# Optimization experiments

Measured on AMD Instinct MI355X. Metric: run time of the kernel, lower is better.

Reference implementation:

```python
import jax, jax.numpy as jnp
import numpy as np

INPUT_DIM = 512
EMBED_DIM = 64
B, S = 4, 4096


def setup_inputs() -> dict:
    key = jax.random.key(0)
    ks = jax.random.split(key, 9)
    scale = 1.0 / np.sqrt(INPUT_DIM)
    return {
        "q": jax.random.normal(ks[0], (B, S, INPUT_DIM), dtype=jnp.float32),
        "k": jax.random.normal(ks[1], (B, S, INPUT_DIM), dtype=jnp.float32),
        "v": jax.random.normal(ks[2], (B, S, INPUT_DIM), dtype=jnp.float32),
        "Wq": jax.random.uniform(ks[3], (INPUT_DIM, EMBED_DIM), jnp.float32, -scale, scale),
        "bq": jax.random.uniform(ks[4], (EMBED_DIM,), jnp.float32, -scale, scale),
        "Wk": jax.random.uniform(ks[5], (INPUT_DIM, EMBED_DIM), jnp.float32, -scale, scale),
        "bk": jax.random.uniform(ks[6], (EMBED_DIM,), jnp.float32, -scale, scale),
        "Wv": jax.random.uniform(ks[7], (INPUT_DIM, EMBED_DIM), jnp.float32, -scale, scale),
        "bv": jax.random.uniform(ks[8], (EMBED_DIM,), jnp.float32, -scale, scale),
    }


def reference(q, k, v, Wq, bq, Wk, bk, Wv, bv):
    # Linear projections (torch Linear: x @ W^T + b; here W stored as [in, out])
    Q = q @ Wq + bq  # [B, S, E]
    K = k @ Wk + bk  # [B, S, E]
    V = v @ Wv + bv  # [B, S, E]
    d_k = K.shape[-1]
    scores = jnp.einsum("bqe,bke->bqk", Q, K) / jnp.sqrt(jnp.float32(d_k))  # [B, S, S]
    attn = jax.nn.softmax(scores, axis=-1)
    return jnp.einsum("bqk,bke->bqe", attn, V)  # [B, S, E]
```

## Files before the change

### kernel.cpp

```cpp
#include <hip/hip_runtime.h>
#include <math.h>

#define S_ 4096
#define C_SCALE 0.18033688011112042f
#define KSPLIT 8

typedef __attribute__((ext_vector_type(4))) float  floatx4;
typedef __attribute__((ext_vector_type(4))) short  short4_t;
typedef __attribute__((ext_vector_type(8))) short  short8_t;
typedef __attribute__((ext_vector_type(4))) unsigned int uintx4;

__device__ __forceinline__ short f2bf(float f) {
  unsigned u = __builtin_bit_cast(unsigned, f);
  u += 0x7FFFu + ((u >> 16) & 1u);
  return (short)(u >> 16);
}
__device__ __forceinline__ unsigned pack2(float lo, float hi) {
  unsigned a = __builtin_bit_cast(unsigned, lo) + 0x8000u;
  unsigned b = __builtin_bit_cast(unsigned, hi) + 0x8000u;
  return __builtin_amdgcn_perm(b, a, 0x07060302u);
}
__device__ __forceinline__ unsigned packt(float lo, float hi) {
  return __builtin_amdgcn_perm(__builtin_bit_cast(unsigned, hi),
                               __builtin_bit_cast(unsigned, lo), 0x07060302u);
}
__device__ __forceinline__ float bf2f(short s) {
  return __builtin_bit_cast(float, (unsigned)((unsigned short)s) << 16);
}

__global__ __launch_bounds__(256) void prep_w(const float* __restrict__ Wq,
                                              const float* __restrict__ Wk,
                                              const float* __restrict__ Wv,
                                              short* __restrict__ Wt) {
  __shared__ float T[64 * 65];
  int m = blockIdx.x >> 3, kt = blockIdx.x & 7, tid = threadIdx.x;
  const float* W = (m == 0) ? Wq : (m == 1) ? Wk : Wv;
  float sc = (m == 0) ? C_SCALE : 1.0f;
#pragma unroll
  for (int i = 0; i < 16; i++) {
    int e = i * 256 + tid;
    int k = e >> 6, n = e & 63;
    T[k * 65 + n] = W[(kt * 64 + k) * 64 + n];
  }
  __syncthreads();
#pragma unroll
  for (int i = 0; i < 16; i++) {
    int e = i * 256 + tid;
    int n = e >> 6, k = e & 63;
    Wt[m * 32768 + n * 512 + kt * 64 + k] = f2bf(T[k * 65 + n] * sc);
  }
}

__global__ __launch_bounds__(256, 3) void proj_kernel(
    const float* __restrict__ qin, const float* __restrict__ kin,
    const float* __restrict__ vin, const float* __restrict__ bq,
    const float* __restrict__ bk, const float* __restrict__ bv,
    const short* __restrict__ Wt, short* __restrict__ Qp,
    short* __restrict__ Kp, short* __restrict__ Vt) {
  __shared__ short A_lds[2][64 * 64];

  int tid = threadIdx.x;
  int m = blockIdx.x >> 8;
  int r0 = (blockIdx.x & 255) * 64;
  int wid = tid >> 6, lane = tid & 63, l15 = lane & 15, quad = lane >> 4;

  const float* in = (m == 0) ? qin : (m == 1) ? kin : vin;
  const short* Wm = Wt + m * 32768;

  short8_t wf[8][2];
#pragma unroll
  for (int kc = 0; kc < 8; kc++)
#pragma unroll
    for (int eh = 0; eh < 2; eh++)
      wf[kc][eh] = *(const short8_t*)(Wm + (wid * 16 + l15) * 512 + kc * 64 +
                                      eh * 32 + quad * 8);

  int sr = tid >> 3, sc = tid & 7;
  int sphys = (sc ^ (sr & 7)) * 8;

  floatx4 ar[4];
  auto loadA = [&](int kc) {
    const float* p = in + (size_t)(r0 + sr) * 512 + kc * 64 + sc * 8;
    ar[0] = *(const floatx4*)p;
    ar[1] = *(const floatx4*)(p + 4);
    const float* p2 = p + 32 * 512;
    ar[2] = *(const floatx4*)p2;
    ar[3] = *(const floatx4*)(p2 + 4);
  };

  floatx4 acc[4];
#pragma unroll
  for (int rt = 0; rt < 4; rt++) acc[rt] = (floatx4){0.f, 0.f, 0.f, 0.f};

  loadA(0);
#pragma unroll
  for (int kc = 0; kc < 8; kc++) {
    uintx4 w0 = {pack2(ar[0][0], ar[0][1]), pack2(ar[0][2], ar[0][3]),
                 pack2(ar[1][0], ar[1][1]), pack2(ar[1][2], ar[1][3])};
    uintx4 w1 = {pack2(ar[2][0], ar[2][1]), pack2(ar[2][2], ar[2][3]),
                 pack2(ar[3][0], ar[3][1]), pack2(ar[3][2], ar[3][3])};
    short* Ab = &A_lds[kc & 1][0];
    *(short8_t*)(Ab + sr * 64 + sphys) = __builtin_bit_cast(short8_t, w0);
    *(short8_t*)(Ab + (sr + 32) * 64 + sphys) = __builtin_bit_cast(short8_t, w1);
    __syncthreads();
    if (kc < 7) loadA(kc + 1);
    int akey = l15 & 7;
#pragma unroll
    for (int rt = 0; rt < 4; rt++) {
      int arow = rt * 16 + l15;
#pragma unroll
      for (int eh = 0; eh < 2; eh++) {
        short8_t af = *(const short8_t*)(Ab + arow * 64 + ((eh * 4 + quad) ^ akey) * 8);
        acc[rt] = __builtin_amdgcn_mfma_f32_16x16x32_bf16(af, wf[kc][eh], acc[rt], 0, 0, 0);
      }
    }
  }

  const float* bias = (m == 0) ? bq : (m == 1) ? bk : bv;
  float bsc = (m == 0) ? C_SCALE : 1.0f;
  float bv_ = bias[wid * 16 + l15] * bsc;
  if (m < 2) {
    short* out = (m == 0) ? Qp : Kp;
#pragma unroll
    for (int rt = 0; rt < 4; rt++)
#pragma unroll
      for (int r = 0; r < 4; r++)
        out[(size_t)(r0 + rt * 16 + quad * 4 + r) * 64 + wid * 16 + l15] =
            f2bf(acc[rt][r] + bv_);
  } else {
    int bb = r0 >> 12;
    int s0 = (r0 & 4095);
#pragma unroll
    for (int rt = 0; rt < 4; rt++) {
      short4_t pk = {f2bf(acc[rt][0] + bv_), f2bf(acc[rt][1] + bv_),
                     f2bf(acc[rt][2] + bv_), f2bf(acc[rt][3] + bv_)};
      *(short4_t*)(Vt + (size_t)bb * 262144 + (wid * 16 + l15) * 4096 + s0 +
                   rt * 16 + quad * 4) = pk;
    }
  }
}

__global__ __launch_bounds__(256, 2) void attn_kernel(
    const short* __restrict__ Qp, const short* __restrict__ Kp,
    const short* __restrict__ Vt, short* __restrict__ Po,
    float* __restrict__ Lp) {
  __shared__ short K_lds[2][64 * 64];
  __shared__ short V_lds[2][64 * 64];

  int tid = threadIdx.x;
  int ks = blockIdx.x >> 6, b = (blockIdx.x >> 4) & 3, qt = blockIdx.x & 15;
  int wid = tid >> 6, lane = tid & 63, l15 = lane & 15, quad = lane >> 4;

  const short* Qb = Qp + (size_t)b * (S_ * 64);
  const short* Kb = Kp + (size_t)b * (S_ * 64);
  const short* Vb = Vt + (size_t)b * (64 * S_);

  int q0 = qt * 256 + wid * 64;

  short8_t qf[4][2];
#pragma unroll
  for (int qs = 0; qs < 4; qs++)
#pragma unroll
    for (int h = 0; h < 2; h++)
      qf[qs][h] = *(const short8_t*)(Qb + (q0 + qs * 16 + l15) * 64 + h * 32 + quad * 8);

  floatx4 o[4][4];
  floatx4 ol[4];
#pragma unroll
  for (int qs = 0; qs < 4; qs++) {
    ol[qs] = (floatx4){0.f, 0.f, 0.f, 0.f};
#pragma unroll
    for (int eb = 0; eb < 4; eb++) o[qs][eb] = (floatx4){0.f, 0.f, 0.f, 0.f};
  }

  short8_t ones;
#pragma unroll
  for (int i = 0; i < 8; i++) ones[i] = (short)0x3F80;

  int sr = tid >> 3, sc = tid & 7;
  int kk = (sr & 3) | (((sr >> 3) & 1) << 2);
  int vk = sr & 7;
  short8_t kr0, kr1, vr0, vr1;
  int ks_base = ks * 512;

  auto loadKV = [&](int t) {
    int ks0 = ks_base + t * 64;
    kr0 = *(const short8_t*)(Kb + (ks0 + sr) * 64 + sc * 8);
    kr1 = *(const short8_t*)(Kb + (ks0 + sr + 32) * 64 + sc * 8);
    vr0 = *(const short8_t*)(Vb + (size_t)sr * 4096 + ks0 + sc * 8);
    vr1 = *(const short8_t*)(Vb + (size_t)(sr + 32) * 4096 + ks0 + sc * 8);
  };
  auto writeKV = [&](int buf) {
    *(short8_t*)(&K_lds[buf][sr * 64 + ((sc ^ kk) * 8)]) = kr0;
    *(short8_t*)(&K_lds[buf][(sr + 32) * 64 + ((sc ^ kk) * 8)]) = kr1;
    *(short8_t*)(&V_lds[buf][sr * 64 + ((sc ^ vk) * 8)]) = vr0;
    *(short8_t*)(&V_lds[buf][(sr + 32) * 64 + ((sc ^ vk) * 8)]) = vr1;
  };

  int pr = 8 * (l15 >> 2) + (l15 & 3);
  int kkey = (l15 & 3) | (((l15 >> 2) & 1) << 2);
  int vkey = l15 & 7;

  loadKV(0);
#pragma unroll
  for (int t = 0; t < 8; t++) {
    writeKV(t & 1);
    __syncthreads();
    if (t < 7) loadKV(t + 1);
    const short* Kt = &K_lds[t & 1][0];
    const short* Vl = &V_lds[t & 1][0];

#pragma unroll
    for (int jg = 0; jg < 2; jg++) {
      const short* Kg = Kt + (jg * 32 + pr) * 64;
      short8_t kA0 = *(const short8_t*)(Kg + ((0 + quad) ^ kkey) * 8);
      short8_t kA1 = *(const short8_t*)(Kg + ((4 + quad) ^ kkey) * 8);
      short8_t kA2 = *(const short8_t*)(Kg + 256 + ((0 + quad) ^ kkey) * 8);
      short8_t kA3 = *(const short8_t*)(Kg + 256 + ((4 + quad) ^ kkey) * 8);
      short8_t vf[4];
#pragma unroll
      for (int eb = 0; eb < 4; eb++)
        vf[eb] = *(const short8_t*)(Vl + (eb * 16 + l15) * 64 +
                                    ((jg * 4 + quad) ^ vkey) * 8);
#pragma unroll
      for (int qs = 0; qs < 4; qs++) {
        floatx4 z = (floatx4){0.f, 0.f, 0.f, 0.f};
        floatx4 s0 = __builtin_amdgcn_mfma_f32_16x16x32_bf16(kA0, qf[qs][0], z, 0, 0, 0);
        s0 = __builtin_amdgcn_mfma_f32_16x16x32_bf16(kA1, qf[qs][1], s0, 0, 0, 0);
        floatx4 s1 = __builtin_amdgcn_mfma_f32_16x16x32_bf16(kA2, qf[qs][0], z, 0, 0, 0);
        s1 = __builtin_amdgcn_mfma_f32_16x16x32_bf16(kA3, qf[qs][1], s1, 0, 0, 0);
        float e00 = __builtin_amdgcn_exp2f(s0[0]), e01 = __builtin_amdgcn_exp2f(s0[1]);
        float e02 = __builtin_amdgcn_exp2f(s0[2]), e03 = __builtin_amdgcn_exp2f(s0[3]);
        float e10 = __builtin_amdgcn_exp2f(s1[0]), e11 = __builtin_amdgcn_exp2f(s1[1]);
        float e12 = __builtin_amdgcn_exp2f(s1[2]), e13 = __builtin_amdgcn_exp2f(s1[3]);
        uintx4 bp = {packt(e00, e01), packt(e02, e03),
                     packt(e10, e11), packt(e12, e13)};
        short8_t pB = __builtin_bit_cast(short8_t, bp);
#pragma unroll
        for (int eb = 0; eb < 4; eb++)
          o[qs][eb] = __builtin_amdgcn_mfma_f32_16x16x32_bf16(vf[eb], pB, o[qs][eb], 0, 0, 0);
        ol[qs] = __builtin_amdgcn_mfma_f32_16x16x32_bf16(ones, pB, ol[qs], 0, 0, 0);
      }
    }
  }

#pragma unroll
  for (int qs = 0; qs < 4; qs++) {
    int grow = b * 4096 + q0 + qs * 16 + l15;
    short* Pb = Po + ((size_t)ks * 16384 + grow) * 64;
#pragma unroll
    for (int eb = 0; eb < 4; eb++) {
      short4_t pk = {f2bf(o[qs][eb][0]), f2bf(o[qs][eb][1]),
                     f2bf(o[qs][eb][2]), f2bf(o[qs][eb][3])};
      *(short4_t*)(Pb + eb * 16 + quad * 4) = pk;
    }
    if (quad == 0) Lp[ks * 16384 + grow] = ol[qs][0];
  }
}

__global__ __launch_bounds__(256) void combine_kernel(
    const short* __restrict__ Po, const float* __restrict__ Lp,
    float* __restrict__ out) {
  int gid = blockIdx.x * 256 + threadIdx.x;
  int grow = gid >> 3, e0 = (gid & 7) * 8;
  float s[8];
#pragma unroll
  for (int i = 0; i < 8; i++) s[i] = 0.f;
  float l = 0.f;
#pragma unroll
  for (int ks = 0; ks < KSPLIT; ks++) {
    short8_t p = *(const short8_t*)(Po + ((size_t)ks * 16384 + grow) * 64 + e0);
#pragma unroll
    for (int i = 0; i < 8; i++) s[i] += bf2f(p[i]);
    l += Lp[ks * 16384 + grow];
  }
  float inv = 1.0f / l;
  floatx4 o0 = {s[0] * inv, s[1] * inv, s[2] * inv, s[3] * inv};
  floatx4 o1 = {s[4] * inv, s[5] * inv, s[6] * inv, s[7] * inv};
  *(floatx4*)(out + (size_t)grow * 64 + e0) = o0;
  *(floatx4*)(out + (size_t)grow * 64 + e0 + 4) = o1;
}

extern "C" void kernel_launch(void* const* d_in, const int* in_sizes, int n_in,
                              void* d_out, int out_size, void* d_ws, size_t ws_size,
                              hipStream_t stream) {
  const float* q = (const float*)d_in[0];
  const float* k = (const float*)d_in[1];
  const float* v = (const float*)d_in[2];
  const float* Wq = (const float*)d_in[3];
  const float* bq = (const float*)d_in[4];
  const float* Wk = (const float*)d_in[5];
  const float* bk = (const float*)d_in[6];
  const float* Wv = (const float*)d_in[7];
  const float* bv = (const float*)d_in[8];

  char* ws = (char*)d_ws;
  short* Qp = (short*)(ws);
  short* Kp = (short*)(ws + (1u << 21));
  short* Vt = (short*)(ws + (2u << 21));
  short* Wt = (short*)(ws + (3u << 21));
  short* Po = (short*)(ws + (4u << 21));
  float* Lp = (float*)(ws + (13u << 21));

  prep_w<<<24, 256, 0, stream>>>(Wq, Wk, Wv, Wt);
  proj_kernel<<<768, 256, 0, stream>>>(q, k, v, bq, bk, bv, Wt, Qp, Kp, Vt);
  attn_kernel<<<512, 256, 0, stream>>>(Qp, Kp, Vt, Po, Lp);
  combine_kernel<<<512, 256, 0, stream>>>(Po, Lp, (float*)d_out);
}
```

Baseline: 168.3 us.

## Load projection A-operands directly into registers with triple-buffered prefetch, drop LDS

The projection kernel stops staging fp32 input tiles through shared memory with barriers. Each lane now loads the exact row and k-slice it feeds to the MFMA straight from global memory, and three slots of loads stay in flight across the 16 k-steps. This removes the LDS writes, LDS reads and __syncthreads. In exchange, every wave re-reads the same 64 input rows, global access is less coalesced (32-byte pieces per lane), and register pressure rises, so launch bounds drop from 3 to 2 blocks per SM.

```diff
diff --git a/kernel.cpp b/kernel.cpp
--- a/kernel.cpp
+++ b/kernel.cpp
@@ -51,14 +51,12 @@
   }
 }
 
-__global__ __launch_bounds__(256, 3) void proj_kernel(
+__global__ __launch_bounds__(256, 2) void proj_kernel(
     const float* __restrict__ qin, const float* __restrict__ kin,
     const float* __restrict__ vin, const float* __restrict__ bq,
     const float* __restrict__ bk, const float* __restrict__ bv,
     const short* __restrict__ Wt, short* __restrict__ Qp,
     short* __restrict__ Kp, short* __restrict__ Vt) {
-  __shared__ short A_lds[2][64 * 64];
-
   int tid = threadIdx.x;
   int m = blockIdx.x >> 8;
   int r0 = (blockIdx.x & 255) * 64;
@@ -67,53 +65,45 @@
   const float* in = (m == 0) ? qin : (m == 1) ? kin : vin;
   const short* Wm = Wt + m * 32768;
 
-  short8_t wf[8][2];
-#pragma unroll
-  for (int kc = 0; kc < 8; kc++)
-#pragma unroll
-    for (int eh = 0; eh < 2; eh++)
-      wf[kc][eh] = *(const short8_t*)(Wm + (wid * 16 + l15) * 512 + kc * 64 +
-                                      eh * 32 + quad * 8);
-
-  int sr = tid >> 3, sc = tid & 7;
-  int sphys = (sc ^ (sr & 7)) * 8;
-
-  floatx4 ar[4];
-  auto loadA = [&](int kc) {
-    const float* p = in + (size_t)(r0 + sr) * 512 + kc * 64 + sc * 8;
-    ar[0] = *(const floatx4*)p;
-    ar[1] = *(const floatx4*)(p + 4);
-    const float* p2 = p + 32 * 512;
-    ar[2] = *(const floatx4*)p2;
-    ar[3] = *(const floatx4*)(p2 + 4);
+  short8_t wf[16];
+#pragma unroll
+  for (int s = 0; s < 16; s++)
+    wf[s] = *(const short8_t*)(Wm + (wid * 16 + l15) * 512 + s * 32 + quad * 8);
+
+  const float* ab = in + (size_t)(r0 + l15) * 512 + quad * 8;
+
+  floatx4 abuf[3][8];
+  auto loadS = [&](int s, int slot) {
+#pragma unroll
+    for (int rt = 0; rt < 4; rt++) {
+      const float* p = ab + (size_t)rt * (16 * 512) + s * 32;
+      abuf[slot][rt * 2] = *(const floatx4*)p;
+      abuf[slot][rt * 2 + 1] = *(const floatx4*)(p + 4);
+    }
   };
 
   floatx4 acc[4];
 #pragma unroll
   for (int rt = 0; rt < 4; rt++) acc[rt] = (floatx4){0.f, 0.f, 0.f, 0.f};
 
-  loadA(0);
-#pragma unroll
-  for (int kc = 0; kc < 8; kc++) {
-    uintx4 w0 = {pack2(ar[0][0], ar[0][1]), pack2(ar[0][2], ar[0][3]),
-                 pack2(ar[1][0], ar[1][1]), pack2(ar[1][2], ar[1][3])};
-    uintx4 w1 = {pack2(ar[2][0], ar[2][1]), pack2(ar[2][2], ar[2][3]),
-                 pack2(ar[3][0], ar[3][1]), pack2(ar[3][2], ar[3][3])};
-    short* Ab = &A_lds[kc & 1][0];
-    *(short8_t*)(Ab + sr * 64 + sphys) = __builtin_bit_cast(short8_t, w0);
-    *(short8_t*)(Ab + (sr + 32) * 64 + sphys) = __builtin_bit_cast(short8_t, w1);
-    __syncthreads();
-    if (kc < 7) loadA(kc + 1);
-    int akey = l15 & 7;
+  loadS(0, 0);
+  loadS(1, 1);
+  loadS(2, 2);
+#pragma unroll
+  for (int s = 0; s < 16; s++) {
+    int slot = s % 3;
+    short8_t af[4];
 #pragma unroll
     for (int rt = 0; rt < 4; rt++) {
-      int arow = rt * 16 + l15;
-#pragma unroll
-      for (int eh = 0; eh < 2; eh++) {
-        short8_t af = *(const short8_t*)(Ab + arow * 64 + ((eh * 4 + quad) ^ akey) * 8);
-        acc[rt] = __builtin_amdgcn_mfma_f32_16x16x32_bf16(af, wf[kc][eh], acc[rt], 0, 0, 0);
-      }
-    }
+      floatx4 a0 = abuf[slot][rt * 2], a1 = abuf[slot][rt * 2 + 1];
+      uintx4 pk = {pack2(a0[0], a0[1]), pack2(a0[2], a0[3]),
+                   pack2(a1[0], a1[1]), pack2(a1[2], a1[3])};
+      af[rt] = __builtin_bit_cast(short8_t, pk);
+    }
+    if (s + 3 < 16) loadS(s + 3, slot);
+#pragma unroll
+    for (int rt = 0; rt < 4; rt++)
+      acc[rt] = __builtin_amdgcn_mfma_f32_16x16x32_bf16(af[rt], wf[s], acc[rt], 0, 0, 0);
   }
 
   const float* bias = (m == 0) ? bq : (m == 1) ? bk : bv;
```

Measured after the change: 190.2 us. 1.13x slower.
